# Kernel optimization log

Hardware: AMD Instinct MI355X
Metric: run time of the kernel (lower is better)

The kernel has to match this reference:

```python
import jax, jax.numpy as jnp
import numpy as np

N_NODES = 100000
N_EDGES = 1600000
D_FEAT = 64


def setup_inputs() -> dict:
    key = jax.random.key(0)
    k1, k2, k3, k4 = jax.random.split(key, 4)
    rows = jnp.sort(jax.random.randint(k1, (N_EDGES,), 0, N_NODES, dtype=jnp.int64))
    cols = jax.random.randint(k2, (N_EDGES,), 0, N_NODES, dtype=jnp.int64)
    vals = jax.random.uniform(k3, (N_EDGES,), dtype=jnp.float32)
    embeds = jax.random.normal(k4, (N_NODES, D_FEAT), dtype=jnp.float32)
    return {"rows": rows, "cols": cols, "vals": vals, "embeds": embeds}


def reference(rows, cols, vals, embeds):
    # out[i] = sum_{e: rows[e]==i} vals[e] * embeds[cols[e]]  (torch.spmm with COO adj)
    gathered = vals[:, None] * embeds[cols]          # [E, d]
    out = jax.ops.segment_sum(gathered, rows, num_segments=N_NODES)  # [N, d]
    return out
```

## Files before the change

### kernel.cpp

```cpp
#include <hip/hip_runtime.h>
#include <hip/hip_bf16.h>


constexpr int D = 64;

__device__ __forceinline__ unsigned bf16rnd(unsigned u) {
    return (u + 0x7FFFu + ((u >> 16) & 1u)) >> 16;
}

__global__ __launch_bounds__(256) void prep_kernel(
    const uint4* __restrict__ src,
    uint4* __restrict__ dst,
    int n8,
    const int* __restrict__ rows, int* __restrict__ row_ptr,
    int n_edges, int n_nodes, int cvt_blocks)
{
    if ((int)blockIdx.x < cvt_blocks) {
        int i = blockIdx.x * 256 + threadIdx.x;
        if (i >= n8) return;
        uint4 a = src[2 * i];
        uint4 b = src[2 * i + 1];
        uint4 o;
        o.x = bf16rnd(a.x) | (bf16rnd(a.y) << 16);
        o.y = bf16rnd(a.z) | (bf16rnd(a.w) << 16);
        o.z = bf16rnd(b.x) | (bf16rnd(b.y) << 16);
        o.w = bf16rnd(b.z) | (bf16rnd(b.w) << 16);
        dst[i] = o;
    } else {
        int e = (blockIdx.x - cvt_blocks) * 256 + threadIdx.x;
        if (e >= n_edges) return;
        int r_cur  = rows[e];
        int r_prev = (e == 0) ? -1 : rows[e - 1];
        for (int r = r_prev + 1; r <= r_cur; ++r) row_ptr[r] = e;
        if (e == n_edges - 1)
            for (int r = r_cur + 1; r <= n_nodes; ++r) row_ptr[r] = n_edges;
    }
}

__device__ __forceinline__ float bflo(unsigned w) {
    union { unsigned u; float f; } x; x.u = w << 16; return x.f;
}
__device__ __forceinline__ float bfhi(unsigned w) {
    union { unsigned u; float f; } x; x.u = w & 0xFFFF0000u; return x.f;
}

__global__ __launch_bounds__(256) void spmm_node_kernel(
    const int* __restrict__ row_ptr,
    const int* __restrict__ cols,
    const float* __restrict__ vals,
    const uint4* __restrict__ ebf4,
    float4* __restrict__ out4,
    int n_nodes)
{
    constexpr int CHUNK = 256;
    __shared__ int   s_cols[4][CHUNK];
    __shared__ float s_vals[4][CHUNK];

    const int lane = threadIdx.x & 63;
    const int t    = lane & 7;
    const int s    = lane >> 3;
    const int w    = threadIdx.x >> 6;
    const int wave = blockIdx.x * (blockDim.x >> 6) + w;
    const int node = wave * 8 + s;
    if (node >= n_nodes) return;

    const int nb    = wave * 8;
    const int nbhi  = (nb + 8 <= n_nodes) ? nb + 8 : n_nodes;
    const int wbase = row_ptr[nb];
    const int wend  = row_ptr[nbhi];
    const int lo    = row_ptr[node];
    const int hi    = row_ptr[node + 1];

    float4 acc0 = make_float4(0.f, 0.f, 0.f, 0.f);
    float4 acc1 = make_float4(0.f, 0.f, 0.f, 0.f);

    for (int cbase = wbase; cbase < wend; cbase += CHUNK) {
        #pragma unroll
        for (int j = 0; j < CHUNK; j += 64) {
            if (cbase + j >= wend) break;
            int idx = cbase + j + lane;
            if (idx < wend) {
                s_cols[w][j + lane] = cols[idx];
                s_vals[w][j + lane] = vals[idx];
            }
        }
        __builtin_amdgcn_wave_barrier();

        const int cend = (cbase + CHUNK < wend) ? cbase + CHUNK : wend;
        int e0 = (lo > cbase) ? lo : cbase;
        int e1 = (hi < cend)  ? hi : cend;

        for (int e = e0; e < e1; e += 4) {
            const int last = e1 - 1;
            int i0 = e - cbase;
            int i1 = ((e + 1 <= last) ? e + 1 : last) - cbase;
            int i2 = ((e + 2 <= last) ? e + 2 : last) - cbase;
            int i3 = ((e + 3 <= last) ? e + 3 : last) - cbase;

            int c0 = s_cols[w][i0], c1 = s_cols[w][i1];
            int c2 = s_cols[w][i2], c3 = s_cols[w][i3];

            float v0 = s_vals[w][i0];
            float v1 = (e + 1 < e1) ? s_vals[w][i1] : 0.f;
            float v2 = (e + 2 < e1) ? s_vals[w][i2] : 0.f;
            float v3 = (e + 3 < e1) ? s_vals[w][i3] : 0.f;

            uint4 m0 = ebf4[c0 * 8 + t];
            uint4 m1 = ebf4[c1 * 8 + t];
            uint4 m2 = ebf4[c2 * 8 + t];
            uint4 m3 = ebf4[c3 * 8 + t];

            acc0.x += v0 * bflo(m0.x); acc0.y += v0 * bfhi(m0.x);
            acc0.z += v0 * bflo(m0.y); acc0.w += v0 * bfhi(m0.y);
            acc1.x += v0 * bflo(m0.z); acc1.y += v0 * bfhi(m0.z);
            acc1.z += v0 * bflo(m0.w); acc1.w += v0 * bfhi(m0.w);

            acc0.x += v1 * bflo(m1.x); acc0.y += v1 * bfhi(m1.x);
            acc0.z += v1 * bflo(m1.y); acc0.w += v1 * bfhi(m1.y);
            acc1.x += v1 * bflo(m1.z); acc1.y += v1 * bfhi(m1.z);
            acc1.z += v1 * bflo(m1.w); acc1.w += v1 * bfhi(m1.w);

            acc0.x += v2 * bflo(m2.x); acc0.y += v2 * bfhi(m2.x);
            acc0.z += v2 * bflo(m2.y); acc0.w += v2 * bfhi(m2.y);
            acc1.x += v2 * bflo(m2.z); acc1.y += v2 * bfhi(m2.z);
            acc1.z += v2 * bflo(m2.w); acc1.w += v2 * bfhi(m2.w);

            acc0.x += v3 * bflo(m3.x); acc0.y += v3 * bfhi(m3.x);
            acc0.z += v3 * bflo(m3.y); acc0.w += v3 * bfhi(m3.y);
            acc1.x += v3 * bflo(m3.z); acc1.y += v3 * bfhi(m3.z);
            acc1.z += v3 * bflo(m3.w); acc1.w += v3 * bfhi(m3.w);
        }
        __builtin_amdgcn_wave_barrier();
    }

    long ob = (long)node * 16 + 2 * t;
    out4[ob]     = acc0;
    out4[ob + 1] = acc1;
}

extern "C" void kernel_launch(void* const* d_in, const int* in_sizes, int n_in,
                              void* d_out, int out_size, void* d_ws, size_t ws_size,
                              hipStream_t stream) {
    const int*   rows   = (const int*)d_in[0];
    const int*   cols   = (const int*)d_in[1];
    const float* vals   = (const float*)d_in[2];
    const float* embeds = (const float*)d_in[3];
    float4*      out4   = (float4*)d_out;

    const int n_edges = in_sizes[0];
    const int n_nodes = out_size / D;
    const int n_feat  = in_sizes[3];

    char*  ws        = (char*)d_ws;
    uint4* ebf_table = (uint4*)ws;
    int*   row_ptr   = (int*)(ws + (size_t)n_feat * 2);

    int n8         = n_feat / 8;
    int cvt_blocks = (n8 + 255) / 256;
    int row_blocks = (n_edges + 255) / 256;
    prep_kernel<<<cvt_blocks + row_blocks, 256, 0, stream>>>(
        (const uint4*)embeds, ebf_table, n8,
        rows, row_ptr, n_edges, n_nodes, cvt_blocks);

    int waves  = (n_nodes + 7) / 8;
    int blocks = (waves + 3) / 4;
    spmm_node_kernel<<<blocks, 256, 0, stream>>>(
        row_ptr, cols, vals, ebf_table, out4, n_nodes);
}
```

Measured before the change: 120.6 us.

## Drop prep kernel: binary-search row bounds and gather fp32 embeddings directly

```diff
diff --git a/kernel.cpp b/kernel.cpp
--- a/kernel.cpp
+++ b/kernel.cpp
@@ -1,78 +1,43 @@
 #include <hip/hip_runtime.h>
-#include <hip/hip_bf16.h>
 
 
 constexpr int D = 64;
 
-__device__ __forceinline__ unsigned bf16rnd(unsigned u) {
-    return (u + 0x7FFFu + ((u >> 16) & 1u)) >> 16;
-}
-
-__global__ __launch_bounds__(256) void prep_kernel(
-    const uint4* __restrict__ src,
-    uint4* __restrict__ dst,
-    int n8,
-    const int* __restrict__ rows, int* __restrict__ row_ptr,
-    int n_edges, int n_nodes, int cvt_blocks)
-{
-    if ((int)blockIdx.x < cvt_blocks) {
-        int i = blockIdx.x * 256 + threadIdx.x;
-        if (i >= n8) return;
-        uint4 a = src[2 * i];
-        uint4 b = src[2 * i + 1];
-        uint4 o;
-        o.x = bf16rnd(a.x) | (bf16rnd(a.y) << 16);
-        o.y = bf16rnd(a.z) | (bf16rnd(a.w) << 16);
-        o.z = bf16rnd(b.x) | (bf16rnd(b.y) << 16);
-        o.w = bf16rnd(b.z) | (bf16rnd(b.w) << 16);
-        dst[i] = o;
-    } else {
-        int e = (blockIdx.x - cvt_blocks) * 256 + threadIdx.x;
-        if (e >= n_edges) return;
-        int r_cur  = rows[e];
-        int r_prev = (e == 0) ? -1 : rows[e - 1];
-        for (int r = r_prev + 1; r <= r_cur; ++r) row_ptr[r] = e;
-        if (e == n_edges - 1)
-            for (int r = r_cur + 1; r <= n_nodes; ++r) row_ptr[r] = n_edges;
-    }
-}
-
-__device__ __forceinline__ float bflo(unsigned w) {
-    union { unsigned u; float f; } x; x.u = w << 16; return x.f;
-}
-__device__ __forceinline__ float bfhi(unsigned w) {
-    union { unsigned u; float f; } x; x.u = w & 0xFFFF0000u; return x.f;
-}
-
-__global__ __launch_bounds__(256) void spmm_node_kernel(
-    const int* __restrict__ row_ptr,
+__global__ __launch_bounds__(256, 4) void spmm_f32_kernel(
+    const int* __restrict__ rows,
     const int* __restrict__ cols,
     const float* __restrict__ vals,
-    const uint4* __restrict__ ebf4,
+    const float4* __restrict__ emb4,
     float4* __restrict__ out4,
-    int n_nodes)
+    int n_edges, int n_nodes)
 {
     constexpr int CHUNK = 256;
     __shared__ int   s_cols[4][CHUNK];
     __shared__ float s_vals[4][CHUNK];
 
     const int lane = threadIdx.x & 63;
-    const int t    = lane & 7;
-    const int s    = lane >> 3;
+    const int t    = lane & 15;
+    const int s    = lane >> 4;
     const int w    = threadIdx.x >> 6;
-    const int wave = blockIdx.x * (blockDim.x >> 6) + w;
-    const int node = wave * 8 + s;
-    if (node >= n_nodes) return;
+    const int wave = blockIdx.x * 4 + w;
+    const int nb   = wave * 4;
+    if (nb >= n_nodes) return;
 
-    const int nb    = wave * 8;
-    const int nbhi  = (nb + 8 <= n_nodes) ? nb + 8 : n_nodes;
-    const int wbase = row_ptr[nb];
-    const int wend  = row_ptr[nbhi];
-    const int lo    = row_ptr[node];
-    const int hi    = row_ptr[node + 1];
+    int target = nb + (lane < 4 ? lane : 4);
+    if (target > n_nodes) target = n_nodes;
+    int sl = 0, sh = n_edges;
+    while (sl < sh) {
+        int mid = (sl + sh) >> 1;
+        if (rows[mid] < target) sl = mid + 1; else sh = mid;
+    }
+    const int wbase = __shfl(sl, 0);
+    const int wend  = __shfl(sl, 4);
+    const int lo    = __shfl(sl, s);
+    const int hi    = __shfl(sl, s + 1);
+    const int node  = nb + s;
+    const bool live = (node < n_nodes);
 
-    float4 acc0 = make_float4(0.f, 0.f, 0.f, 0.f);
-    float4 acc1 = make_float4(0.f, 0.f, 0.f, 0.f);
+    float4 acc = make_float4(0.f, 0.f, 0.f, 0.f);
 
     for (int cbase = wbase; cbase < wend; cbase += CHUNK) {
         #pragma unroll
@@ -90,52 +55,70 @@
         int e0 = (lo > cbase) ? lo : cbase;
         int e1 = (hi < cend)  ? hi : cend;
 
-        for (int e = e0; e < e1; e += 4) {
+        for (int e = e0; e < e1; e += 8) {
             const int last = e1 - 1;
             int i0 = e - cbase;
             int i1 = ((e + 1 <= last) ? e + 1 : last) - cbase;
             int i2 = ((e + 2 <= last) ? e + 2 : last) - cbase;
             int i3 = ((e + 3 <= last) ? e + 3 : last) - cbase;
+            int i4 = ((e + 4 <= last) ? e + 4 : last) - cbase;
+            int i5 = ((e + 5 <= last) ? e + 5 : last) - cbase;
+            int i6 = ((e + 6 <= last) ? e + 6 : last) - cbase;
+            int i7 = ((e + 7 <= last) ? e + 7 : last) - cbase;
 
             int c0 = s_cols[w][i0], c1 = s_cols[w][i1];
             int c2 = s_cols[w][i2], c3 = s_cols[w][i3];
+            int c4 = s_cols[w][i4], c5 = s_cols[w][i5];
+            int c6 = s_cols[w][i6], c7 = s_cols[w][i7];
 
             float v0 = s_vals[w][i0];
             float v1 = (e + 1 < e1) ? s_vals[w][i1] : 0.f;
             float v2 = (e + 2 < e1) ? s_vals[w][i2] : 0.f;
             float v3 = (e + 3 < e1) ? s_vals[w][i3] : 0.f;
+            float v4 = (e + 4 < e1) ? s_vals[w][i4] : 0.f;
+            float v5 = (e + 5 < e1) ? s_vals[w][i5] : 0.f;
+            float v6 = (e + 6 < e1) ? s_vals[w][i6] : 0.f;
+            float v7 = (e + 7 < e1) ? s_vals[w][i7] : 0.f;
 
-            uint4 m0 = ebf4[c0 * 8 + t];
-            uint4 m1 = ebf4[c1 * 8 + t];
-            uint4 m2 = ebf4[c2 * 8 + t];
-            uint4 m3 = ebf4[c3 * 8 + t];
+            float4 m0 = emb4[c0 * 16 + t];
+            float4 m1 = emb4[c1 * 16 + t];
+            float4 m2 = emb4[c2 * 16 + t];
+            float4 m3 = emb4[c3 * 16 + t];
+            float4 m4 = emb4[c4 * 16 + t];
+            float4 m5 = emb4[c5 * 16 + t];
+            float4 m6 = emb4[c6 * 16 + t];
+            float4 m7 = emb4[c7 * 16 + t];
 
-            acc0.x += v0 * bflo(m0.x); acc0.y += v0 * bfhi(m0.x);
-            acc0.z += v0 * bflo(m0.y); acc0.w += v0 * bfhi(m0.y);
-            acc1.x += v0 * bflo(m0.z); acc1.y += v0 * bfhi(m0.z);
-            acc1.z += v0 * bflo(m0.w); acc1.w += v0 * bfhi(m0.w);
+            acc.x += v0 * m0.x; acc.y += v0 * m0.y;
+            acc.z += v0 * m0.z; acc.w += v0 * m0.w;
 
-            acc0.x += v1 * bflo(m1.x); acc0.y += v1 * bfhi(m1.x);
-            acc0.z += v1 * bflo(m1.y); acc0.w += v1 * bfhi(m1.y);
-            acc1.x += v1 * bflo(m1.z); acc1.y += v1 * bfhi(m1.z);
-            acc1.z += v1 * bflo(m1.w); acc1.w += v1 * bfhi(m1.w);
+            acc.x += v1 * m1.x; acc.y += v1 * m1.y;
+            acc.z += v1 * m1.z; acc.w += v1 * m1.w;
 
-            acc0.x += v2 * bflo(m2.x); acc0.y += v2 * bfhi(m2.x);
-            acc0.z += v2 * bflo(m2.y); acc0.w += v2 * bfhi(m2.y);
-            acc1.x += v2 * bflo(m2.z); acc1.y += v2 * bfhi(m2.z);
-            acc1.z += v2 * bflo(m2.w); acc1.w += v2 * bfhi(m2.w);
+            acc.x += v2 * m2.x; acc.y += v2 * m2.y;
+            acc.z += v2 * m2.z; acc.w += v2 * m2.w;
 
-            acc0.x += v3 * bflo(m3.x); acc0.y += v3 * bfhi(m3.x);
-            acc0.z += v3 * bflo(m3.y); acc0.w += v3 * bfhi(m3.y);
-            acc1.x += v3 * bflo(m3.z); acc1.y += v3 * bfhi(m3.z);
-            acc1.z += v3 * bflo(m3.w); acc1.w += v3 * bfhi(m3.w);
+            acc.x += v3 * m3.x; acc.y += v3 * m3.y;
+            acc.z += v3 * m3.z; acc.w += v3 * m3.w;
+
+            acc.x += v4 * m4.x; acc.y += v4 * m4.y;
+            acc.z += v4 * m4.z; acc.w += v4 * m4.w;
+
+            acc.x += v5 * m5.x; acc.y += v5 * m5.y;
+            acc.z += v5 * m5.z; acc.w += v5 * m5.w;
+
+            acc.x += v6 * m6.x; acc.y += v6 * m6.y;
+            acc.z += v6 * m6.z; acc.w += v6 * m6.w;
+
+            acc.x += v7 * m7.x; acc.y += v7 * m7.y;
+            acc.z += v7 * m7.z; acc.w += v7 * m7.w;
         }
         __builtin_amdgcn_wave_barrier();
     }
 
-    long ob = (long)node * 16 + 2 * t;
-    out4[ob]     = acc0;
-    out4[ob + 1] = acc1;
+    if (live) {
+        out4[(long)node * 16 + t] = acc;
+    }
 }
 
 extern "C" void kernel_launch(void* const* d_in, const int* in_sizes, int n_in,
@@ -149,21 +132,11 @@
 
     const int n_edges = in_sizes[0];
     const int n_nodes = out_size / D;
-    const int n_feat  = in_sizes[3];
 
-    char*  ws        = (char*)d_ws;
-    uint4* ebf_table = (uint4*)ws;
-    int*   row_ptr   = (int*)(ws + (size_t)n_feat * 2);
+    (void)d_ws; (void)ws_size; (void)n_in;
 
-    int n8         = n_feat / 8;
-    int cvt_blocks = (n8 + 255) / 256;
-    int row_blocks = (n_edges + 255) / 256;
-    prep_kernel<<<cvt_blocks + row_blocks, 256, 0, stream>>>(
-        (const uint4*)embeds, ebf_table, n8,
-        rows, row_ptr, n_edges, n_nodes, cvt_blocks);
-
-    int waves  = (n_nodes + 7) / 8;
+    int waves  = (n_nodes + 3) / 4;
     int blocks = (waves + 3) / 4;
-    spmm_node_kernel<<<blocks, 256, 0, stream>>>(
-        row_ptr, cols, vals, ebf_table, out4, n_nodes);
+    spmm_f32_kernel<<<blocks, 256, 0, stream>>>(
+        rows, cols, vals, (const float4*)embeds, out4, n_edges, n_nodes);
 }
```

New measurement: 149.1 us. +23.6%, slower.

## Transpose bf16 embedding table into feature slices and split SpMM per slice

Applied to the files above, without the earlier changes.

```diff
diff --git a/kernel.cpp b/kernel.cpp
--- a/kernel.cpp
+++ b/kernel.cpp
@@ -1,23 +1,31 @@
 #include <hip/hip_runtime.h>
-#include <hip/hip_bf16.h>
 
 
 constexpr int D = 64;
 
+typedef float v4f __attribute__((ext_vector_type(4)));
+
 __device__ __forceinline__ unsigned bf16rnd(unsigned u) {
     return (u + 0x7FFFu + ((u >> 16) & 1u)) >> 16;
+}
+__device__ __forceinline__ float bflo(unsigned w) {
+    union { unsigned u; float f; } x; x.u = w << 16; return x.f;
+}
+__device__ __forceinline__ float bfhi(unsigned w) {
+    union { unsigned u; float f; } x; x.u = w & 0xFFFF0000u; return x.f;
 }
 
 __global__ __launch_bounds__(256) void prep_kernel(
     const uint4* __restrict__ src,
-    uint4* __restrict__ dst,
-    int n8,
+    uint4* __restrict__ dstT,
+    int n8, int n_nodes,
     const int* __restrict__ rows, int* __restrict__ row_ptr,
-    int n_edges, int n_nodes, int cvt_blocks)
+    int n_edges, int cvt_blocks)
 {
     if ((int)blockIdx.x < cvt_blocks) {
         int i = blockIdx.x * 256 + threadIdx.x;
         if (i >= n8) return;
+        int c = i >> 3, k = i & 7;
         uint4 a = src[2 * i];
         uint4 b = src[2 * i + 1];
         uint4 o;
@@ -25,7 +33,7 @@
         o.y = bf16rnd(a.z) | (bf16rnd(a.w) << 16);
         o.z = bf16rnd(b.x) | (bf16rnd(b.y) << 16);
         o.w = bf16rnd(b.z) | (bf16rnd(b.w) << 16);
-        dst[i] = o;
+        dstT[(size_t)k * n_nodes + c] = o;
     } else {
         int e = (blockIdx.x - cvt_blocks) * 256 + threadIdx.x;
         if (e >= n_edges) return;
@@ -37,18 +45,11 @@
     }
 }
 
-__device__ __forceinline__ float bflo(unsigned w) {
-    union { unsigned u; float f; } x; x.u = w << 16; return x.f;
-}
-__device__ __forceinline__ float bfhi(unsigned w) {
-    union { unsigned u; float f; } x; x.u = w & 0xFFFF0000u; return x.f;
-}
-
-__global__ __launch_bounds__(256) void spmm_node_kernel(
+__global__ __launch_bounds__(256, 4) void spmm_slice_kernel(
     const int* __restrict__ row_ptr,
     const int* __restrict__ cols,
     const float* __restrict__ vals,
-    const uint4* __restrict__ ebf4,
+    const uint4* __restrict__ ebfT,
     float4* __restrict__ out4,
     int n_nodes)
 {
@@ -57,85 +58,107 @@
     __shared__ float s_vals[4][CHUNK];
 
     const int lane = threadIdx.x & 63;
-    const int t    = lane & 7;
+    const int j    = lane & 7;
     const int s    = lane >> 3;
     const int w    = threadIdx.x >> 6;
-    const int wave = blockIdx.x * (blockDim.x >> 6) + w;
-    const int node = wave * 8 + s;
-    if (node >= n_nodes) return;
+    const int k    = blockIdx.x & 7;
+    const int p    = blockIdx.x >> 3;
+    const int nb   = p * 32 + w * 8;
+    if (nb >= n_nodes) return;
 
-    const int nb    = wave * 8;
+    const uint4* __restrict__ slice = ebfT + (size_t)k * n_nodes;
+
     const int nbhi  = (nb + 8 <= n_nodes) ? nb + 8 : n_nodes;
     const int wbase = row_ptr[nb];
     const int wend  = row_ptr[nbhi];
-    const int lo    = row_ptr[node];
-    const int hi    = row_ptr[node + 1];
+    const int node  = nb + s;
+    const bool live = (node < n_nodes);
+    const int lo    = live ? row_ptr[node]     : wend;
+    const int hi    = live ? row_ptr[node + 1] : wend;
 
     float4 acc0 = make_float4(0.f, 0.f, 0.f, 0.f);
     float4 acc1 = make_float4(0.f, 0.f, 0.f, 0.f);
 
     for (int cbase = wbase; cbase < wend; cbase += CHUNK) {
         #pragma unroll
-        for (int j = 0; j < CHUNK; j += 64) {
-            if (cbase + j >= wend) break;
-            int idx = cbase + j + lane;
+        for (int q = 0; q < CHUNK; q += 64) {
+            if (cbase + q >= wend) break;
+            int idx = cbase + q + lane;
             if (idx < wend) {
-                s_cols[w][j + lane] = cols[idx];
-                s_vals[w][j + lane] = vals[idx];
+                s_cols[w][q + lane] = __builtin_nontemporal_load(&cols[idx]);
+                s_vals[w][q + lane] = __builtin_nontemporal_load(&vals[idx]);
             }
         }
         __builtin_amdgcn_wave_barrier();
 
         const int cend = (cbase + CHUNK < wend) ? cbase + CHUNK : wend;
-        int e0 = (lo > cbase) ? lo : cbase;
-        int e1 = (hi < cend)  ? hi : cend;
+        const int e0 = (lo > cbase) ? lo : cbase;
+        const int e1 = (hi < cend)  ? hi : cend;
 
-        for (int e = e0; e < e1; e += 4) {
+        for (int e = e0 + j; e < e1; e += 32) {
             const int last = e1 - 1;
-            int i0 = e - cbase;
-            int i1 = ((e + 1 <= last) ? e + 1 : last) - cbase;
-            int i2 = ((e + 2 <= last) ? e + 2 : last) - cbase;
-            int i3 = ((e + 3 <= last) ? e + 3 : last) - cbase;
+            int ia = e;
+            int ib = (e + 8  <= last) ? e + 8  : last;
+            int ic = (e + 16 <= last) ? e + 16 : last;
+            int id = (e + 24 <= last) ? e + 24 : last;
 
-            int c0 = s_cols[w][i0], c1 = s_cols[w][i1];
-            int c2 = s_cols[w][i2], c3 = s_cols[w][i3];
+            int ca = s_cols[w][ia - cbase];
+            int cb = s_cols[w][ib - cbase];
+            int cc = s_cols[w][ic - cbase];
+            int cd = s_cols[w][id - cbase];
 
-            float v0 = s_vals[w][i0];
-            float v1 = (e + 1 < e1) ? s_vals[w][i1] : 0.f;
-            float v2 = (e + 2 < e1) ? s_vals[w][i2] : 0.f;
-            float v3 = (e + 3 < e1) ? s_vals[w][i3] : 0.f;
+            float va = s_vals[w][ia - cbase];
+            float vb = (e + 8  < e1) ? s_vals[w][ib - cbase] : 0.f;
+            float vc = (e + 16 < e1) ? s_vals[w][ic - cbase] : 0.f;
+            float vd = (e + 24 < e1) ? s_vals[w][id - cbase] : 0.f;
 
-            uint4 m0 = ebf4[c0 * 8 + t];
-            uint4 m1 = ebf4[c1 * 8 + t];
-            uint4 m2 = ebf4[c2 * 8 + t];
-            uint4 m3 = ebf4[c3 * 8 + t];
+            uint4 ma = slice[ca];
+            uint4 mb = slice[cb];
+            uint4 mc = slice[cc];
+            uint4 md = slice[cd];
 
-            acc0.x += v0 * bflo(m0.x); acc0.y += v0 * bfhi(m0.x);
-            acc0.z += v0 * bflo(m0.y); acc0.w += v0 * bfhi(m0.y);
-            acc1.x += v0 * bflo(m0.z); acc1.y += v0 * bfhi(m0.z);
-            acc1.z += v0 * bflo(m0.w); acc1.w += v0 * bfhi(m0.w);
+            acc0.x += va * bflo(ma.x); acc0.y += va * bfhi(ma.x);
+            acc0.z += va * bflo(ma.y); acc0.w += va * bfhi(ma.y);
+            acc1.x += va * bflo(ma.z); acc1.y += va * bfhi(ma.z);
+            acc1.z += va * bflo(ma.w); acc1.w += va * bfhi(ma.w);
 
-            acc0.x += v1 * bflo(m1.x); acc0.y += v1 * bfhi(m1.x);
-            acc0.z += v1 * bflo(m1.y); acc0.w += v1 * bfhi(m1.y);
-            acc1.x += v1 * bflo(m1.z); acc1.y += v1 * bfhi(m1.z);
-            acc1.z += v1 * bflo(m1.w); acc1.w += v1 * bfhi(m1.w);
+            acc0.x += vb * bflo(mb.x); acc0.y += vb * bfhi(mb.x);
+            acc0.z += vb * bflo(mb.y); acc0.w += vb * bfhi(mb.y);
+            acc1.x += vb * bflo(mb.z); acc1.y += vb * bfhi(mb.z);
+            acc1.z += vb * bflo(mb.w); acc1.w += vb * bfhi(mb.w);
 
-            acc0.x += v2 * bflo(m2.x); acc0.y += v2 * bfhi(m2.x);
-            acc0.z += v2 * bflo(m2.y); acc0.w += v2 * bfhi(m2.y);
-            acc1.x += v2 * bflo(m2.z); acc1.y += v2 * bfhi(m2.z);
-            acc1.z += v2 * bflo(m2.w); acc1.w += v2 * bfhi(m2.w);
+            acc0.x += vc * bflo(mc.x); acc0.y += vc * bfhi(mc.x);
+            acc0.z += vc * bflo(mc.y); acc0.w += vc * bfhi(mc.y);
+            acc1.x += vc * bflo(mc.z); acc1.y += vc * bfhi(mc.z);
+            acc1.z += vc * bflo(mc.w); acc1.w += vc * bfhi(mc.w);
 
-            acc0.x += v3 * bflo(m3.x); acc0.y += v3 * bfhi(m3.x);
-            acc0.z += v3 * bflo(m3.y); acc0.w += v3 * bfhi(m3.y);
-            acc1.x += v3 * bflo(m3.z); acc1.y += v3 * bfhi(m3.z);
-            acc1.z += v3 * bflo(m3.w); acc1.w += v3 * bfhi(m3.w);
+            acc0.x += vd * bflo(md.x); acc0.y += vd * bfhi(md.x);
+            acc0.z += vd * bflo(md.y); acc0.w += vd * bfhi(md.y);
+            acc1.x += vd * bflo(md.z); acc1.y += vd * bfhi(md.z);
+            acc1.z += vd * bflo(md.w); acc1.w += vd * bfhi(md.w);
         }
         __builtin_amdgcn_wave_barrier();
     }
 
-    long ob = (long)node * 16 + 2 * t;
-    out4[ob]     = acc0;
-    out4[ob + 1] = acc1;
+    #pragma unroll
+    for (int m = 1; m <= 4; m <<= 1) {
+        acc0.x += __shfl_xor(acc0.x, m, 64);
+        acc0.y += __shfl_xor(acc0.y, m, 64);
+        acc0.z += __shfl_xor(acc0.z, m, 64);
+        acc0.w += __shfl_xor(acc0.w, m, 64);
+        acc1.x += __shfl_xor(acc1.x, m, 64);
+        acc1.y += __shfl_xor(acc1.y, m, 64);
+        acc1.z += __shfl_xor(acc1.z, m, 64);
+        acc1.w += __shfl_xor(acc1.w, m, 64);
+    }
+
+    if (live) {
+        long ob = (long)node * 16 + k * 2;
+        if (j == 0)
+            __builtin_nontemporal_store(*(const v4f*)&acc0, (v4f*)&out4[ob]);
+        if (j == 1)
+            __builtin_nontemporal_store(*(const v4f*)&acc1, (v4f*)&out4[ob + 1]);
+    }
 }
 
 extern "C" void kernel_launch(void* const* d_in, const int* in_sizes, int n_in,
@@ -152,18 +175,18 @@
     const int n_feat  = in_sizes[3];
 
     char*  ws        = (char*)d_ws;
-    uint4* ebf_table = (uint4*)ws;
+    uint4* ebfT      = (uint4*)ws;
     int*   row_ptr   = (int*)(ws + (size_t)n_feat * 2);
 
     int n8         = n_feat / 8;
     int cvt_blocks = (n8 + 255) / 256;
     int row_blocks = (n_edges + 255) / 256;
     prep_kernel<<<cvt_blocks + row_blocks, 256, 0, stream>>>(
-        (const uint4*)embeds, ebf_table, n8,
-        rows, row_ptr, n_edges, n_nodes, cvt_blocks);
+        (const uint4*)embeds, ebfT, n8, n_nodes,
+        rows, row_ptr, n_edges, cvt_blocks);
 
-    int waves  = (n_nodes + 7) / 8;
-    int blocks = (waves + 3) / 4;
-    spmm_node_kernel<<<blocks, 256, 0, stream>>>(
-        row_ptr, cols, vals, ebf_table, out4, n_nodes);
+    int parts  = (n_nodes + 31) / 32;
+    int blocks = parts * 8;
+    spmm_slice_kernel<<<blocks, 256, 0, stream>>>(
+        row_ptr, cols, vals, ebfT, out4, n_nodes);
 }
```

Result: slower. 209.8 us (+73.9%).
